# Performance work log

Hardware: AMD Instinct MI355X
Metric: run time of the kernel (lower is better)

Reference implementation:

```python
import jax, jax.numpy as jnp
import numpy as np

EMB = 1024
HID = 1024

def setup_inputs() -> dict:
    key = jax.random.key(0)
    k1, k2, k3, k4, k5 = jax.random.split(key, 5)
    s_ih = 1.0 / np.sqrt(HID)
    embeds = jax.random.normal(k1, (64, 512, EMB), dtype=jnp.float32)
    W_ih = jax.random.uniform(k2, (HID, EMB), jnp.float32, -s_ih, s_ih)
    W_hh = jax.random.uniform(k3, (HID, HID), jnp.float32, -s_ih, s_ih)
    b_ih = jax.random.uniform(k4, (HID,), jnp.float32, -s_ih, s_ih)
    b_hh = jax.random.uniform(k5, (HID,), jnp.float32, -s_ih, s_ih)
    return {"embeds": embeds, "W_ih": W_ih, "W_hh": W_hh, "b_ih": b_ih, "b_hh": b_hh}

def reference(embeds, W_ih, W_hh, b_ih, b_hh):
    # Elman RNN with tanh: h_t = tanh(x_t W_ih^T + b_ih + h_{t-1} W_hh^T + b_hh)
    B, S, _ = embeds.shape
    # Precompute input projection for all timesteps in one big GEMM: (B,S,H)
    x_proj = jnp.einsum('bse,he->bsh', embeds, W_ih) + b_ih + b_hh
    h0 = jnp.zeros((B, W_hh.shape[0]), dtype=embeds.dtype)

    def step(h, xp_t):
        h_new = jnp.tanh(xp_t + h @ W_hh.T)
        return h_new, h_new

    # scan over time axis: inputs (S,B,H)
    _, hs = jax.lax.scan(step, h0, jnp.swapaxes(x_proj, 0, 1))
    return hs  # (S, B, H): hidden state at each timestep
```

## Files before the change

### kernel.cpp

```cpp
#include <hip/hip_runtime.h>
#include <math.h>

#define EMB    1024
#define HID    1024
#define BATCH    64
#define SEQ     512

#define NBG     16
#define BTILE    4
#define NJT     16
#define JTILE   64

#define SLOT   65536
#define STEPSZ 65536

typedef float f32x4 __attribute__((ext_vector_type(4)));

__global__ __launch_bounds__(256) void xproj_gemm(
    const float* __restrict__ A,
    const float* __restrict__ W,
    const float* __restrict__ b_ih,
    const float* __restrict__ b_hh,
    float* __restrict__ out)
{
    __shared__ float As[16][68];
    __shared__ float Ws[16][68];

    const int tid = threadIdx.x;
    const int tx  = tid & 15;
    const int ty  = tid >> 4;
    const int m0  = blockIdx.y * 64;
    const int n0  = blockIdx.x * 64;
    const int lrow = tid >> 2;
    const int lk   = (tid & 3) * 4;

    float acc[4][4] = {};

    for (int kt = 0; kt < EMB; kt += 16) {
        float4 av = *(const float4*)&A[(size_t)(m0 + lrow) * EMB + kt + lk];
        float4 wv = *(const float4*)&W[(size_t)(n0 + lrow) * EMB + kt + lk];
        As[lk + 0][lrow] = av.x; As[lk + 1][lrow] = av.y;
        As[lk + 2][lrow] = av.z; As[lk + 3][lrow] = av.w;
        Ws[lk + 0][lrow] = wv.x; Ws[lk + 1][lrow] = wv.y;
        Ws[lk + 2][lrow] = wv.z; Ws[lk + 3][lrow] = wv.w;
        __syncthreads();
        #pragma unroll
        for (int kk = 0; kk < 16; ++kk) {
            float4 a = *(const float4*)&As[kk][ty * 4];
            float4 w = *(const float4*)&Ws[kk][tx * 4];
            acc[0][0] += a.x * w.x; acc[0][1] += a.x * w.y;
            acc[0][2] += a.x * w.z; acc[0][3] += a.x * w.w;
            acc[1][0] += a.y * w.x; acc[1][1] += a.y * w.y;
            acc[1][2] += a.y * w.z; acc[1][3] += a.y * w.w;
            acc[2][0] += a.z * w.x; acc[2][1] += a.z * w.y;
            acc[2][2] += a.z * w.z; acc[2][3] += a.z * w.w;
            acc[3][0] += a.w * w.x; acc[3][1] += a.w * w.y;
            acc[3][2] += a.w * w.z; acc[3][3] += a.w * w.w;
        }
        __syncthreads();
    }

    const int n = n0 + tx * 4;
    float bias[4];
    #pragma unroll
    for (int j = 0; j < 4; ++j) bias[j] = b_ih[n + j] + b_hh[n + j];

    #pragma unroll
    for (int i = 0; i < 4; ++i) {
        const int m = m0 + ty * 4 + i;
        const int b = m >> 9;
        const int s = m & 511;
        float4 o;
        o.x = acc[i][0] + bias[0];
        o.y = acc[i][1] + bias[1];
        o.z = acc[i][2] + bias[2];
        o.w = acc[i][3] + bias[3];
        *(float4*)&out[((size_t)(s * 64 + b) << 10) + n] = o;
    }
}

__device__ __forceinline__ float red16(float x) {
    int xi, yi;
    xi = __builtin_bit_cast(int, x);
    yi = __builtin_amdgcn_update_dpp(0, xi, 0xB1, 0xF, 0xF, true);
    x += __builtin_bit_cast(float, yi);
    xi = __builtin_bit_cast(int, x);
    yi = __builtin_amdgcn_update_dpp(0, xi, 0x4E, 0xF, 0xF, true);
    x += __builtin_bit_cast(float, yi);
    xi = __builtin_bit_cast(int, x);
    yi = __builtin_amdgcn_update_dpp(0, xi, 0x124, 0xF, 0xF, true);
    x += __builtin_bit_cast(float, yi);
    xi = __builtin_bit_cast(int, x);
    yi = __builtin_amdgcn_update_dpp(0, xi, 0x128, 0xF, 0xF, true);
    x += __builtin_bit_cast(float, yi);
    return x;
}

__device__ __forceinline__ f32x4 llc_load4_async(const float* p) {
    f32x4 v;
    asm volatile("global_load_dwordx4 %0, %1, off sc1"
                 : "=&v"(v) : "v"(p) : "memory");
    return v;
}

__device__ __forceinline__ f32x4 llc_load4_sync(const float* p) {
    f32x4 v;
    asm volatile("global_load_dwordx4 %0, %1, off sc1\n\t"
                 "s_waitcnt vmcnt(0)"
                 : "=&v"(v) : "v"(p) : "memory");
    return v;
}

__device__ __forceinline__ void wait_vm0() {
    asm volatile("s_waitcnt vmcnt(0)" ::: "memory");
    __builtin_amdgcn_sched_barrier(0);
}

__device__ __forceinline__ void bar_lgkm() {
    asm volatile("s_waitcnt lgkmcnt(0)\n\ts_barrier" ::: "memory");
}

__device__ __forceinline__ bool inrange4(f32x4 v, float lo, float hi) {
    return v.x >= lo && v.x <= hi && v.y >= lo && v.y <= hi &&
           v.z >= lo && v.z <= hi && v.w >= lo && v.w <= hi;
}

__global__ __launch_bounds__(512, 2) void rnn_persist(
    const float* __restrict__ Whh,
    float* __restrict__ out,
    float* __restrict__ exch)
{
    const int tid  = threadIdx.x;
    const int wave = tid >> 6;
    const int lane = tid & 63;
    const int c    = lane & 15;
    const int jt   = blockIdx.x;
    const int bg   = blockIdx.y;
    const int jbase = jt * JTILE + wave * 8 + ((lane >> 4) & 3) * 2;
    const int k0    = c * 64;

    f32x4 wr0[16], wr1[16];
    #pragma unroll
    for (int kq = 0; kq < 16; ++kq) {
        wr0[kq] = *(const f32x4*)&Whh[(size_t)jbase * HID + k0 + kq * 4];
        wr1[kq] = *(const f32x4*)&Whh[(size_t)(jbase + 1) * HID + k0 + kq * 4];
    }
    #pragma unroll
    for (int kq = 0; kq < 16; ++kq) {
        asm volatile("" : "+v"(wr0[kq]));
        asm volatile("" : "+v"(wr1[kq]));
    }

    __shared__ float hsf[2 * 1088];

    const bool have  = (tid < 256);
    const int  fidx  = tid & 255;
    const int  ldoff = (fidx >> 4) * 68 + (fidx & 15) * 4;
    const int  gq    = fidx * 4;

    const int jout  = jbase + (c & 1);
    const int mybat = c >> 1;
    const int orow  = (bg * BTILE + mybat) * HID + jout;

    if (c < 8) {
        float h0 = tanhf(out[orow]);
        out[orow] = h0;
        __hip_atomic_store(&exch[orow], h0, __ATOMIC_RELAXED,
                           __HIP_MEMORY_SCOPE_AGENT);
    }

    float xp = 0.f;
    if (c < 8) xp = out[(size_t)STEPSZ + orow];

    f32x4 pf = {0.f, 0.f, 0.f, 0.f};
    if (have) pf = llc_load4_async(exch + (bg * BTILE + 0) * HID + gq);

    float pend = 0.f;

    for (int t = 1; t < SEQ; ++t) {
        #pragma unroll
        for (int b = 0; b < 4; ++b) {
            const int   tp    = t - 1;
            const float off   = 4.0f * (float)(tp & 3);
            const float lo    = off - 1.0f, hi = off + 1.0f;
            const float* ebase = exch + (tp & 1) * SLOT + (bg * BTILE + b) * HID;

            wait_vm0();

            {
                const int bprev = (b == 0) ? 3 : (b - 1);
                const int tprev = (b == 0) ? (t - 1) : t;
                if (!(b == 0 && t == 1)) {
                    if (mybat == bprev) {
                        const int oi = (bg * BTILE + bprev) * HID + jout;
                        out[(size_t)tprev * STEPSZ + oi] = pend;
                        __hip_atomic_store(&exch[(tprev & 1) * SLOT + oi],
                                           pend + 4.0f * (float)(tprev & 3),
                                           __ATOMIC_RELAXED,
                                           __HIP_MEMORY_SCOPE_AGENT);
                    }
                }
            }

            bool ok = !have || inrange4(pf, lo, hi);
            while (!__all(ok)) {
                if (!ok) {
                    pf = llc_load4_sync(ebase + gq);
                    ok = inrange4(pf, lo, hi);
                }
            }

            if (have) *(f32x4*)&hsf[(b & 1) * 1088 + ldoff] = pf - off;

            {
                const int bn = (b + 1) & 3;
                const int tn = (b == 3) ? (t + 1) : t;
                if (tn < SEQ) {
                    const float* nb =
                        exch + ((tn - 1) & 1) * SLOT + (bg * BTILE + bn) * HID;
                    if (have) pf = llc_load4_async(nb + gq);
                }
            }

            bar_lgkm();

            {
                const float* base = &hsf[(b & 1) * 1088 + c * 68];
                f32x4 s0 = {0.f, 0.f, 0.f, 0.f};
                f32x4 s1 = {0.f, 0.f, 0.f, 0.f};
                #pragma unroll
                for (int kq = 0; kq < 16; ++kq) {
                    f32x4 h4 = *(const f32x4*)&base[kq * 4];
                    s0 += h4 * wr0[kq];
                    s1 += h4 * wr1[kq];
                }
                float a0 = (s0.x + s0.y) + (s0.z + s0.w);
                float a1 = (s1.x + s1.y) + (s1.z + s1.w);
                a0 = red16(a0);
                a1 = red16(a1);
                if (mybat == b) {
                    pend = tanhf(xp + ((c & 1) ? a1 : a0));
                }
            }

            if (b == 3 && t + 1 < SEQ) {
                if (c < 8) xp = out[(size_t)(t + 1) * STEPSZ + orow];
            }
        }
    }

    if (mybat == 3) {
        out[(size_t)(SEQ - 1) * STEPSZ + (bg * BTILE + 3) * HID + jout] = pend;
    }
}

extern "C" void kernel_launch(void* const* d_in, const int* in_sizes, int n_in,
                              void* d_out, int out_size, void* d_ws, size_t ws_size,
                              hipStream_t stream) {
    const float* embeds = (const float*)d_in[0];
    const float* W_ih   = (const float*)d_in[1];
    const float* W_hh   = (const float*)d_in[2];
    const float* b_ih   = (const float*)d_in[3];
    const float* b_hh   = (const float*)d_in[4];
    float* out = (float*)d_out;

    (void)in_sizes; (void)n_in; (void)out_size; (void)ws_size;

    hipMemsetAsync(d_ws, 0x7F, 2 * SLOT * sizeof(float), stream);

    dim3 gA(HID / 64, (BATCH * SEQ) / 64);
    xproj_gemm<<<gA, 256, 0, stream>>>(embeds, W_ih, b_ih, b_hh, out);

    dim3 gR(NJT, NBG);
    rnn_persist<<<gR, 512, 0, stream>>>(W_hh, out, (float*)d_ws);
}
```

Before: 2.571 ms.

## Double prefetch depth with 8-batch groups and partial vmcnt waits in persistent RNN

Batch groups now hold 8 batch rows per block instead of 4, so all 16 lanes of a column group own an output and the grid has half as many batch groups. The hidden-state exchange loads are now double-buffered two sub-iterations ahead (pfA/pfB), and waits use vmcnt(5)/vmcnt(1) so outstanding stores and prefetches are not drained each step. Each result is stored and published as soon as it is computed rather than deferred to the next sub-iteration. The flag encoding adds a 16.0 offset that alternates between pairs of batch rows to tell buffers apart. This risks correctness if the vmcnt counts do not match the real number of outstanding memory operations, and each block now does twice the sequential work per timestep.

```diff
diff --git a/kernel.cpp b/kernel.cpp
--- a/kernel.cpp
+++ b/kernel.cpp
@@ -6,8 +6,8 @@
 #define BATCH    64
 #define SEQ     512
 
-#define NBG     16
-#define BTILE    4
+#define NBG      8
+#define BTILE    8
 #define NJT     16
 #define JTILE   64
 
@@ -111,8 +111,12 @@
     return v;
 }
 
-__device__ __forceinline__ void wait_vm0() {
-    asm volatile("s_waitcnt vmcnt(0)" ::: "memory");
+__device__ __forceinline__ void wait_vm5() {
+    asm volatile("s_waitcnt vmcnt(5)" ::: "memory");
+    __builtin_amdgcn_sched_barrier(0);
+}
+__device__ __forceinline__ void wait_vm1() {
+    asm volatile("s_waitcnt vmcnt(1)" ::: "memory");
     __builtin_amdgcn_sched_barrier(0);
 }
 
@@ -124,6 +128,53 @@
     return v.x >= lo && v.x <= hi && v.y >= lo && v.y <= hi &&
            v.z >= lo && v.z <= hi && v.w >= lo && v.w <= hi;
 }
+
+#define SUBITER(BB, WAITFN)                                                   \
+  do {                                                                        \
+    const int   tp  = t - 1;                                                  \
+    const float off = 4.0f * (float)(tp & 3)                                  \
+                    + 16.0f * (float)(((BB) >> 1) & 1);                       \
+    const float lo = off - 1.0f, hi = off + 1.0f;                             \
+    const float* ebase = exch + (tp & 1) * SLOT + (bg * BTILE + (BB)) * HID;  \
+    WAITFN();                                                                 \
+    f32x4& PF = ((BB) & 1) ? pfB : pfA;                                       \
+    bool ok = !have || inrange4(PF, lo, hi);                                  \
+    while (!__all(ok)) {                                                      \
+      if (!ok) { PF = llc_load4_sync(ebase + gq); ok = inrange4(PF, lo, hi); }\
+    }                                                                         \
+    if (have) *(f32x4*)&hsf[((BB) & 1) * 1088 + ldoff] = PF - off;            \
+    {                                                                         \
+      const int bn = ((BB) + 2) & 7;                                          \
+      const int tn = ((BB) >= 6) ? t + 1 : t;                                 \
+      if (tn < SEQ) {                                                         \
+        const float* nb = exch + ((tn - 1) & 1) * SLOT                        \
+                          + (bg * BTILE + bn) * HID;                          \
+        if (have) PF = llc_load4_async(nb + gq);                              \
+      }                                                                       \
+    }                                                                         \
+    bar_lgkm();                                                               \
+    {                                                                         \
+      const float* base = &hsf[((BB) & 1) * 1088 + c * 68];                   \
+      f32x4 s0 = {0.f,0.f,0.f,0.f}, s1 = {0.f,0.f,0.f,0.f};                   \
+      _Pragma("unroll")                                                       \
+      for (int kq = 0; kq < 16; ++kq) {                                       \
+        f32x4 h4 = *(const f32x4*)&base[kq * 4];                              \
+        s0 += h4 * wr0[kq]; s1 += h4 * wr1[kq];                               \
+      }                                                                       \
+      float a0 = (s0.x + s0.y) + (s0.z + s0.w);                               \
+      float a1 = (s1.x + s1.y) + (s1.z + s1.w);                               \
+      a0 = red16(a0); a1 = red16(a1);                                         \
+      if (mybat == (BB)) {                                                    \
+        float hv = tanhf(xp + ((c & 1) ? a1 : a0));                           \
+        out[(size_t)t * STEPSZ + orow] = hv;                                  \
+        __hip_atomic_store(&exch[(t & 1) * SLOT + orow],                      \
+                           hv + 4.0f * (float)(t & 3)                         \
+                              + 16.0f * (float)(((BB) >> 1) & 1),             \
+                           __ATOMIC_RELAXED, __HIP_MEMORY_SCOPE_AGENT);       \
+      }                                                                       \
+    }                                                                         \
+    if ((BB) == 7 && t + 1 < SEQ) xp = out[(size_t)(t + 1) * STEPSZ + orow];  \
+  } while (0)
 
 __global__ __launch_bounds__(512, 2) void rnn_persist(
     const float* __restrict__ Whh,
@@ -162,95 +213,43 @@
     const int mybat = c >> 1;
     const int orow  = (bg * BTILE + mybat) * HID + jout;
 
-    if (c < 8) {
+    {
         float h0 = tanhf(out[orow]);
         out[orow] = h0;
-        __hip_atomic_store(&exch[orow], h0, __ATOMIC_RELAXED,
-                           __HIP_MEMORY_SCOPE_AGENT);
-    }
-
-    float xp = 0.f;
-    if (c < 8) xp = out[(size_t)STEPSZ + orow];
-
-    f32x4 pf = {0.f, 0.f, 0.f, 0.f};
-    if (have) pf = llc_load4_async(exch + (bg * BTILE + 0) * HID + gq);
-
-    float pend = 0.f;
-
-    for (int t = 1; t < SEQ; ++t) {
-        #pragma unroll
-        for (int b = 0; b < 4; ++b) {
-            const int   tp    = t - 1;
-            const float off   = 4.0f * (float)(tp & 3);
-            const float lo    = off - 1.0f, hi = off + 1.0f;
-            const float* ebase = exch + (tp & 1) * SLOT + (bg * BTILE + b) * HID;
-
-            wait_vm0();
-
-            {
-                const int bprev = (b == 0) ? 3 : (b - 1);
-                const int tprev = (b == 0) ? (t - 1) : t;
-                if (!(b == 0 && t == 1)) {
-                    if (mybat == bprev) {
-                        const int oi = (bg * BTILE + bprev) * HID + jout;
-                        out[(size_t)tprev * STEPSZ + oi] = pend;
-                        __hip_atomic_store(&exch[(tprev & 1) * SLOT + oi],
-                                           pend + 4.0f * (float)(tprev & 3),
-                                           __ATOMIC_RELAXED,
-                                           __HIP_MEMORY_SCOPE_AGENT);
-                    }
-                }
-            }
-
-            bool ok = !have || inrange4(pf, lo, hi);
-            while (!__all(ok)) {
-                if (!ok) {
-                    pf = llc_load4_sync(ebase + gq);
-                    ok = inrange4(pf, lo, hi);
-                }
-            }
-
-            if (have) *(f32x4*)&hsf[(b & 1) * 1088 + ldoff] = pf - off;
-
-            {
-                const int bn = (b + 1) & 3;
-                const int tn = (b == 3) ? (t + 1) : t;
-                if (tn < SEQ) {
-                    const float* nb =
-                        exch + ((tn - 1) & 1) * SLOT + (bg * BTILE + bn) * HID;
-                    if (have) pf = llc_load4_async(nb + gq);
-                }
-            }
-
-            bar_lgkm();
-
-            {
-                const float* base = &hsf[(b & 1) * 1088 + c * 68];
-                f32x4 s0 = {0.f, 0.f, 0.f, 0.f};
-                f32x4 s1 = {0.f, 0.f, 0.f, 0.f};
-                #pragma unroll
-                for (int kq = 0; kq < 16; ++kq) {
-                    f32x4 h4 = *(const f32x4*)&base[kq * 4];
-                    s0 += h4 * wr0[kq];
-                    s1 += h4 * wr1[kq];
-                }
-                float a0 = (s0.x + s0.y) + (s0.z + s0.w);
-                float a1 = (s1.x + s1.y) + (s1.z + s1.w);
-                a0 = red16(a0);
-                a1 = red16(a1);
-                if (mybat == b) {
-                    pend = tanhf(xp + ((c & 1) ? a1 : a0));
-                }
-            }
-
-            if (b == 3 && t + 1 < SEQ) {
-                if (c < 8) xp = out[(size_t)(t + 1) * STEPSZ + orow];
-            }
-        }
-    }
-
-    if (mybat == 3) {
-        out[(size_t)(SEQ - 1) * STEPSZ + (bg * BTILE + 3) * HID + jout] = pend;
+        __hip_atomic_store(&exch[orow],
+                           h0 + 16.0f * (float)((c >> 2) & 1),
+                           __ATOMIC_RELAXED, __HIP_MEMORY_SCOPE_AGENT);
+    }
+
+    float xp = out[(size_t)STEPSZ + orow];
+
+    f32x4 pfA = {0.f,0.f,0.f,0.f}, pfB = {0.f,0.f,0.f,0.f};
+    if (have) {
+        pfA = llc_load4_async(exch + (bg * BTILE + 0) * HID + gq);
+        pfB = llc_load4_async(exch + (bg * BTILE + 1) * HID + gq);
+    }
+
+    {
+        const int t = 1;
+        SUBITER(0, wait_vm1);
+        SUBITER(1, wait_vm1);
+        SUBITER(2, wait_vm5);
+        SUBITER(3, wait_vm5);
+        SUBITER(4, wait_vm5);
+        SUBITER(5, wait_vm5);
+        SUBITER(6, wait_vm5);
+        SUBITER(7, wait_vm5);
+    }
+
+    for (int t = 2; t < SEQ; ++t) {
+        SUBITER(0, wait_vm5);
+        SUBITER(1, wait_vm5);
+        SUBITER(2, wait_vm5);
+        SUBITER(3, wait_vm5);
+        SUBITER(4, wait_vm5);
+        SUBITER(5, wait_vm5);
+        SUBITER(6, wait_vm5);
+        SUBITER(7, wait_vm5);
     }
 }
 
```

Measured after the change: 4.000 ms. 1.56x slower.
